# Performance work log

Hardware: AMD Instinct MI355X
Metric: run time of the kernel (lower is better)

The kernel has to match this reference:

```python
import jax, jax.numpy as jnp
import numpy as np

BETA = 0.25

def setup_inputs() -> dict:
    key = jax.random.key(0)
    k1, k2, k3, k4 = jax.random.split(key, 4)
    B, C, H, W = 8, 4, 64, 64
    K = 8192
    return {
        'z_e_in': jax.random.normal(k1, (B, C, H, W), dtype=jnp.float32),
        'pq_w': jax.random.normal(k2, (C, C), dtype=jnp.float32) * 0.5,
        'pq_b': jax.random.normal(k3, (C,), dtype=jnp.float32) * 0.1,
        'codebook': jax.random.normal(k4, (K, C), dtype=jnp.float32),
    }

def reference(z_e_in, pq_w, pq_b, codebook):
    # pre_quant_conv: 1x1 conv == channel-mixing matmul
    z_e = jnp.einsum('bchw,oc->bohw', z_e_in, pq_w) + pq_b[None, :, None, None]
    B, C, H, W = z_e.shape
    z = z_e.transpose(0, 2, 3, 1).reshape(B, H * W, C)  # [B, HW, C]
    # squared Euclidean distances (argmin is invariant to sqrt in torch.cdist)
    d2 = (jnp.sum(z * z, axis=-1, keepdims=True)
          - 2.0 * jnp.einsum('bnc,kc->bnk', z, codebook)
          + jnp.sum(codebook * codebook, axis=-1))  # [B, HW, K]
    idx = jnp.argmin(d2, axis=-1)                    # [B, HW]
    z_q = codebook[idx]                               # gather, [B, HW, C]
    z_flat = z.reshape(-1, C)
    zq_flat = z_q.reshape(-1, C)
    sg = jax.lax.stop_gradient
    commitment_loss = jnp.mean((sg(zq_flat) - z_flat) ** 2)
    codebook_loss = jnp.mean((zq_flat - sg(z_flat)) ** 2)
    q_loss = codebook_loss + BETA * commitment_loss
    # straight-through estimator
    zq_st = z_flat + sg(zq_flat - z_flat)
    latent = zq_st.reshape(B, H, W, C).transpose(0, 3, 1, 2)  # [B, C, H, W]
    return latent, q_loss
```

## Files before the change

kernel.cpp:

```cpp
#include <hip/hip_runtime.h>
#include <math.h>

#define N_POINTS 32768
#define KCODES   8192
#define HW       4096
#define CHW      16384

#define NSEG    64
#define SEGLEN  (KCODES / NSEG)
#define PPT     4
#define BLOCK   512
#define PTILE   (BLOCK * PPT)
#define GRIDX   (N_POINTS / PTILE)

#define WS_PACKED 0

typedef float f2 __attribute__((ext_vector_type(2)));
typedef float f4 __attribute__((ext_vector_type(4)));

static __device__ __forceinline__ f2 pk_mul(f2 a, f2 b) {
  f2 d;
  asm("v_pk_mul_f32 %0, %1, %2" : "=v"(d) : "v"(a), "v"(b));
  return d;
}
static __device__ __forceinline__ f2 pk_add(f2 a, f2 b) {
  f2 d;
  asm("v_pk_add_f32 %0, %1, %2" : "=v"(d) : "v"(a), "v"(b));
  return d;
}

__device__ __forceinline__ void compute_z(
    const float* __restrict__ ze, const float* __restrict__ w,
    const float* __restrict__ bias, int n, float zo[4], float& zz) {
  int b = n >> 12, hw = n & 4095;
  const float* p = ze + b * CHW + hw;
  float x0 = p[0], x1 = p[HW], x2 = p[2 * HW], x3 = p[3 * HW];
#pragma unroll
  for (int o = 0; o < 4; ++o) {
    float acc = __fmul_rn(x0, w[o * 4 + 0]);
    acc = __fadd_rn(acc, __fmul_rn(x1, w[o * 4 + 1]));
    acc = __fadd_rn(acc, __fmul_rn(x2, w[o * 4 + 2]));
    acc = __fadd_rn(acc, __fmul_rn(x3, w[o * 4 + 3]));
    zo[o] = __fadd_rn(acc, bias[o]);
  }
  float s = __fmul_rn(zo[0], zo[0]);
  s = __fadd_rn(s, __fmul_rn(zo[1], zo[1]));
  s = __fadd_rn(s, __fmul_rn(zo[2], zo[2]));
  s = __fadd_rn(s, __fmul_rn(zo[3], zo[3]));
  zz = s;
}

__global__ __launch_bounds__(512, 4) void vq_scan(
    const float* __restrict__ ze, const float* __restrict__ w,
    const float* __restrict__ bias, const float* __restrict__ cb,
    unsigned long long* __restrict__ packed) {
  __shared__ float sm[5][SEGLEN] __attribute__((aligned(16)));
  int tid = threadIdx.x;
  int k0 = blockIdx.y * SEGLEN;

  if (tid < SEGLEN) {
    f4 c = ((const f4*)cb)[k0 + tid];
    sm[0][tid] = __fmul_rn(-2.f, c.x);
    sm[1][tid] = __fmul_rn(-2.f, c.y);
    sm[2][tid] = __fmul_rn(-2.f, c.z);
    sm[3][tid] = __fmul_rn(-2.f, c.w);
    float cn = __fmul_rn(c.x, c.x);
    cn = __fadd_rn(cn, __fmul_rn(c.y, c.y));
    cn = __fadd_rn(cn, __fmul_rn(c.z, c.z));
    cn = __fadd_rn(cn, __fmul_rn(c.w, c.w));
    sm[4][tid] = cn;
  }

  int n0 = blockIdx.x * PTILE + tid;
  f2 zd[PPT][4], zzd[PPT];
  float best[PPT];
  int bidx[PPT];
#pragma unroll
  for (int p = 0; p < PPT; ++p) {
    float z[4], zz;
    compute_z(ze, w, bias, n0 + BLOCK * p, z, zz);
#pragma unroll
    for (int c = 0; c < 4; ++c) zd[p][c] = (f2){z[c], z[c]};
    zzd[p] = (f2){zz, zz};
    best[p] = INFINITY;
    bidx[p] = 0;
  }
  __syncthreads();

#pragma unroll 2
  for (int j = 0; j < SEGLEN; j += 4) {
    f4 q0 = *(const f4*)&sm[0][j];
    f4 q1 = *(const f4*)&sm[1][j];
    f4 q2 = *(const f4*)&sm[2][j];
    f4 q3 = *(const f4*)&sm[3][j];
    f4 qn = *(const f4*)&sm[4][j];
#pragma unroll
    for (int p = 0; p < PPT; ++p) {
      f2 dA = pk_mul(zd[p][0], q0.xy);
      dA = pk_add(dA, pk_mul(zd[p][1], q1.xy));
      dA = pk_add(dA, pk_mul(zd[p][2], q2.xy));
      dA = pk_add(dA, pk_mul(zd[p][3], q3.xy));
      f2 sA = pk_add(pk_add(zzd[p], dA), qn.xy);
      f2 dB = pk_mul(zd[p][0], q0.zw);
      dB = pk_add(dB, pk_mul(zd[p][1], q1.zw));
      dB = pk_add(dB, pk_mul(zd[p][2], q2.zw));
      dB = pk_add(dB, pk_mul(zd[p][3], q3.zw));
      f2 sB = pk_add(pk_add(zzd[p], dB), qn.zw);
      if (sA.x < best[p]) { best[p] = sA.x; bidx[p] = j + 0; }
      if (sA.y < best[p]) { best[p] = sA.y; bidx[p] = j + 1; }
      if (sB.x < best[p]) { best[p] = sB.x; bidx[p] = j + 2; }
      if (sB.y < best[p]) { best[p] = sB.y; bidx[p] = j + 3; }
    }
  }

#pragma unroll
  for (int p = 0; p < PPT; ++p) {
    unsigned int u = __float_as_uint(best[p]);
    unsigned int so = (u & 0x80000000u) ? ~u : (u | 0x80000000u);
    unsigned long long key =
        ((unsigned long long)so << 32) | (unsigned int)(k0 + bidx[p]);
    atomicMin(&packed[n0 + BLOCK * p], key);
  }
}

__global__ __launch_bounds__(256) void vq_finish(
    const float* __restrict__ ze, const float* __restrict__ w,
    const float* __restrict__ bias, const float* __restrict__ cb,
    const unsigned long long* __restrict__ packed, float* __restrict__ out) {
  int n = blockIdx.x * 256 + threadIdx.x;
  int bidx = (unsigned int)(packed[n] & 0xFFFFFFFFull);
  float4 c = ((const float4*)cb)[bidx];
  int b = n >> 12, hw = n & 4095;
  float* o = out + b * CHW + hw;
  o[0] = c.x; o[HW] = c.y; o[2 * HW] = c.z; o[3 * HW] = c.w;
  float z[4], zz;
  compute_z(ze, w, bias, n, z, zz);
  float d0 = c.x - z[0], d1 = c.y - z[1], d2 = c.z - z[2], d3 = c.w - z[3];
  float e = d0 * d0 + d1 * d1 + d2 * d2 + d3 * d3;
#pragma unroll
  for (int off = 32; off > 0; off >>= 1) e += __shfl_down(e, off, 64);
  __shared__ float sred[4];
  if ((threadIdx.x & 63) == 0) sred[threadIdx.x >> 6] = e;
  __syncthreads();
  if (threadIdx.x == 0) {
    float t = (sred[0] + sred[1]) + (sred[2] + sred[3]);
    atomicAdd(out + (N_POINTS * 4), t * (1.25f / 131072.f));
  }
}

extern "C" void kernel_launch(void* const* d_in, const int* in_sizes, int n_in,
                              void* d_out, int out_size, void* d_ws, size_t ws_size,
                              hipStream_t stream) {
  const float* ze   = (const float*)d_in[0];
  const float* w    = (const float*)d_in[1];
  const float* bias = (const float*)d_in[2];
  const float* cb   = (const float*)d_in[3];

  unsigned long long* packed =
      (unsigned long long*)((char*)d_ws + WS_PACKED);
  float* out = (float*)d_out;

  hipMemsetAsync(packed, 0xFF, N_POINTS * sizeof(unsigned long long), stream);
  hipMemsetAsync((char*)d_out + (size_t)N_POINTS * 4 * sizeof(float), 0,
                 sizeof(float), stream);
  vq_scan<<<dim3(GRIDX, NSEG), BLOCK, 0, stream>>>(ze, w, bias, cb, packed);
  vq_finish<<<128, 256, 0, stream>>>(ze, w, bias, cb, packed, out);
}
```

Baseline: 128.8 us.

## Pack two points per packed-FP32 lane and duplicate codebook entries in LDS

The packed multiply-add now runs over two different points against one broadcast codebook entry, instead of one point against two codes. The LDS codebook tile stores each scalar duplicated as a float2. Points per thread double to 8, which halves the x-grid and amortises each LDS read over more points. The cost is more registers for eight running best/index pairs, possibly lower occupancy under the 512x4 launch bound, doubled LDS per block, and fewer blocks in flight.

```diff
diff --git a/kernel.cpp b/kernel.cpp
--- a/kernel.cpp
+++ b/kernel.cpp
@@ -8,7 +8,7 @@
 
 #define NSEG    64
 #define SEGLEN  (KCODES / NSEG)
-#define PPT     4
+#define PPT     8
 #define BLOCK   512
 #define PTILE   (BLOCK * PPT)
 #define GRIDX   (N_POINTS / PTILE)
@@ -54,62 +54,65 @@
     const float* __restrict__ ze, const float* __restrict__ w,
     const float* __restrict__ bias, const float* __restrict__ cb,
     unsigned long long* __restrict__ packed) {
-  __shared__ float sm[5][SEGLEN] __attribute__((aligned(16)));
+  __shared__ f2 sm[5][SEGLEN] __attribute__((aligned(16)));
   int tid = threadIdx.x;
   int k0 = blockIdx.y * SEGLEN;
 
   if (tid < SEGLEN) {
     f4 c = ((const f4*)cb)[k0 + tid];
-    sm[0][tid] = __fmul_rn(-2.f, c.x);
-    sm[1][tid] = __fmul_rn(-2.f, c.y);
-    sm[2][tid] = __fmul_rn(-2.f, c.z);
-    sm[3][tid] = __fmul_rn(-2.f, c.w);
+    float m0 = __fmul_rn(-2.f, c.x), m1 = __fmul_rn(-2.f, c.y);
+    float m2 = __fmul_rn(-2.f, c.z), m3 = __fmul_rn(-2.f, c.w);
     float cn = __fmul_rn(c.x, c.x);
     cn = __fadd_rn(cn, __fmul_rn(c.y, c.y));
     cn = __fadd_rn(cn, __fmul_rn(c.z, c.z));
     cn = __fadd_rn(cn, __fmul_rn(c.w, c.w));
-    sm[4][tid] = cn;
+    sm[0][tid] = (f2){m0, m0};
+    sm[1][tid] = (f2){m1, m1};
+    sm[2][tid] = (f2){m2, m2};
+    sm[3][tid] = (f2){m3, m3};
+    sm[4][tid] = (f2){cn, cn};
   }
 
   int n0 = blockIdx.x * PTILE + tid;
-  f2 zd[PPT][4], zzd[PPT];
+  f2 zd[PPT / 2][4], zzd[PPT / 2];
   float best[PPT];
   int bidx[PPT];
 #pragma unroll
-  for (int p = 0; p < PPT; ++p) {
-    float z[4], zz;
-    compute_z(ze, w, bias, n0 + BLOCK * p, z, zz);
+  for (int i = 0; i < PPT / 2; ++i) {
+    float zA[4], zB[4], zzA, zzB;
+    compute_z(ze, w, bias, n0 + BLOCK * (2 * i),     zA, zzA);
+    compute_z(ze, w, bias, n0 + BLOCK * (2 * i + 1), zB, zzB);
 #pragma unroll
-    for (int c = 0; c < 4; ++c) zd[p][c] = (f2){z[c], z[c]};
-    zzd[p] = (f2){zz, zz};
-    best[p] = INFINITY;
-    bidx[p] = 0;
+    for (int c = 0; c < 4; ++c) zd[i][c] = (f2){zA[c], zB[c]};
+    zzd[i] = (f2){zzA, zzB};
+    best[2 * i] = INFINITY;     bidx[2 * i] = 0;
+    best[2 * i + 1] = INFINITY; bidx[2 * i + 1] = 0;
   }
   __syncthreads();
 
 #pragma unroll 2
-  for (int j = 0; j < SEGLEN; j += 4) {
+  for (int j = 0; j < SEGLEN; j += 2) {
     f4 q0 = *(const f4*)&sm[0][j];
     f4 q1 = *(const f4*)&sm[1][j];
     f4 q2 = *(const f4*)&sm[2][j];
     f4 q3 = *(const f4*)&sm[3][j];
     f4 qn = *(const f4*)&sm[4][j];
 #pragma unroll
-    for (int p = 0; p < PPT; ++p) {
-      f2 dA = pk_mul(zd[p][0], q0.xy);
-      dA = pk_add(dA, pk_mul(zd[p][1], q1.xy));
-      dA = pk_add(dA, pk_mul(zd[p][2], q2.xy));
-      dA = pk_add(dA, pk_mul(zd[p][3], q3.xy));
-      f2 sA = pk_add(pk_add(zzd[p], dA), qn.xy);
-      f2 dB = pk_mul(zd[p][0], q0.zw);
-      dB = pk_add(dB, pk_mul(zd[p][1], q1.zw));
-      dB = pk_add(dB, pk_mul(zd[p][2], q2.zw));
-      dB = pk_add(dB, pk_mul(zd[p][3], q3.zw));
-      f2 sB = pk_add(pk_add(zzd[p], dB), qn.zw);
-      if (sA.x < best[p]) { best[p] = sA.x; bidx[p] = j + 0; }
-      if (sA.y < best[p]) { best[p] = sA.y; bidx[p] = j + 1; }
-      if (sB.x < best[p]) { best[p] = sB.x; bidx[p] = j + 2; }
-      if (sB.y < best[p]) { best[p] = sB.y; bidx[p] = j + 3; }
+    for (int i = 0; i < PPT / 2; ++i) {
+      f2 dA = pk_mul(zd[i][0], q0.xy);
+      dA = pk_add(dA, pk_mul(zd[i][1], q1.xy));
+      dA = pk_add(dA, pk_mul(zd[i][2], q2.xy));
+      dA = pk_add(dA, pk_mul(zd[i][3], q3.xy));
+      f2 sA = pk_add(pk_add(zzd[i], dA), qn.xy);
+      if (sA.x < best[2 * i])     { best[2 * i] = sA.x;     bidx[2 * i] = j; }
+      if (sA.y < best[2 * i + 1]) { best[2 * i + 1] = sA.y; bidx[2 * i + 1] = j; }
+      f2 dB = pk_mul(zd[i][0], q0.zw);
+      dB = pk_add(dB, pk_mul(zd[i][1], q1.zw));
+      dB = pk_add(dB, pk_mul(zd[i][2], q2.zw));
+      dB = pk_add(dB, pk_mul(zd[i][3], q3.zw));
+      f2 sB = pk_add(pk_add(zzd[i], dB), qn.zw);
+      if (sB.x < best[2 * i])     { best[2 * i] = sB.x;     bidx[2 * i] = j + 1; }
+      if (sB.y < best[2 * i + 1]) { best[2 * i + 1] = sB.y; bidx[2 * i + 1] = j + 1; }
     }
   }
 
```

Measured after the change: 133.9 us. 1.04x slower.
